# Performance work log

Measured on AMD Instinct MI355X. Metric: run time of the kernel, lower is better.

Reference implementation:

```python
import jax, jax.numpy as jnp
import numpy as np

STRIDE = 8  # window over x[:, max(0, i-stride) : i+1]


def setup_inputs() -> dict:
    key = jax.random.key(0)
    k0, k1, k2, k3, k4 = jax.random.split(key, 5)
    B, T, H = 16, 8192, 256
    x = jax.random.normal(k0, (B, T, H), dtype=jnp.float32)
    s = 1.0 / np.sqrt(H)  # torch nn.Linear default init range
    W_lin = jax.random.uniform(k1, (H, H), jnp.float32, -s, s)
    b_lin = jax.random.uniform(k2, (H,), jnp.float32, -s, s)
    W_mem = jax.random.uniform(k3, (H, H), jnp.float32, -s, s)
    b_mem = jax.random.uniform(k4, (H,), jnp.float32, -s, s)
    return {"x": x, "W_lin": W_lin, "b_lin": b_lin, "W_mem": W_mem, "b_mem": b_mem}


def reference(x, W_lin, b_lin, W_mem, b_mem):
    # x: [B, T, H]; input_dim == hidden_dim so input_lin is None in the original.
    B, T, H = x.shape
    # h = Linear(x)  (torch Linear: x @ W.T + b)
    h = jnp.einsum('bth,oh->bto', x, W_lin) + b_lin
    # Causal sliding-window mean over window [max(0, t-STRIDE), t] via cumsum.
    cs = jnp.cumsum(x, axis=1)                       # [B, T, H]
    idx = jnp.arange(T)
    start = jnp.maximum(0, idx - STRIDE)             # [T]
    prev = jnp.where((start > 0)[None, :, None],
                     cs[:, jnp.maximum(start - 1, 0)], 0.0)
    counts = (idx - start + 1).astype(x.dtype)       # min(t+1, STRIDE+1)
    means = (cs - prev) / counts[None, :, None]      # [B, T, H]
    # memory branch: Linear over window means, batched as one matmul
    mem = jnp.einsum('bth,oh->bto', means, W_mem) + b_mem
    return h + mem
```

## Files before the change

### kernel.cpp

```cpp
#include <hip/hip_runtime.h>
#include <hip/hip_bf16.h>

#define B_ 16
#define T_ 8192
#define H_ 256
#define M_ (B_ * T_)
#define STRIDE_ 8

typedef __bf16 bf16x8 __attribute__((ext_vector_type(8)));
typedef float f32x4 __attribute__((ext_vector_type(4)));

__device__ __forceinline__ unsigned short f2bf(float f) {
  unsigned u = __builtin_bit_cast(unsigned, f);
  u += 0x7fffu + ((u >> 16) & 1u);
  return (unsigned short)(u >> 16);
}

__global__ __launch_bounds__(256) void wcat_kernel(
    const float* __restrict__ Wl, const float* __restrict__ bl,
    const float* __restrict__ Wm, const float* __restrict__ bm,
    unsigned short* __restrict__ Wpk, float* __restrict__ bias) {
  const int e = blockIdx.x * 256 + threadIdx.x;
  const int ks = e >> 13;
  const int n = (e >> 5) & 255;
  const int kk = e & 31;
  const int k = ks * 32 + kk;
  const float w = (k < 256) ? Wl[n * 256 + k] : Wm[n * 256 + (k - 256)];
  Wpk[e] = f2bf(w);
  if (e < 256) bias[e] = bl[e] + bm[e];
}

__global__ __launch_bounds__(256, 3) void fused_kernel(
    const float* __restrict__ x,
    const unsigned short* __restrict__ Wpk,
    const float* __restrict__ bias,
    float* __restrict__ out) {
  __shared__ __align__(16) unsigned short As[2][64 * 64];
  const int tid = threadIdx.x;
  const int m0 = blockIdx.x << 6;
  const int tb0 = m0 & (T_ - 1);
  const int w = tid >> 6;
  const int l = tid & 63;
  const int wc = w << 6;
  const int lm = l & 15;
  const int kc4 = l >> 4;
  const int kq = kc4 << 3;

  const int p = tid & 15, g = tid >> 4;
  const float2* __restrict__ x2 = (const float2*)x;

  f32x4 acc[4][4];
#pragma unroll
  for (int i = 0; i < 4; ++i)
#pragma unroll
    for (int j = 0; j < 4; ++j) acc[i][j] = (f32x4){0.f, 0.f, 0.f, 0.f};

  float2 v[12];
#pragma unroll
  for (int i = 0; i < 12; ++i) {
    const int rl = (g << 2) - 8 + i;
    float2 val = {0.f, 0.f};
    if (tb0 + rl >= 0) val = x2[(size_t)(m0 + rl) * 128 + p];
    v[i] = val;
  }

  for (int it = 0; it < 8; ++it) {
    const int cur = it & 1;
    unsigned* __restrict__ As32 = (unsigned*)As[cur];

    float sx = 0.f, sy = 0.f;
#pragma unroll
    for (int i = 0; i < 8; ++i) { sx += v[i].x; sy += v[i].y; }
#pragma unroll
    for (int rr = 0; rr < 4; ++rr) {
      sx += v[rr + 8].x; sy += v[rr + 8].y;
      const int r = (g << 2) + rr;
      const int t = tb0 + r;
      const float inv =
          (t >= STRIDE_) ? (1.f / 9.f) : __builtin_amdgcn_rcpf((float)(t + 1));
      const unsigned xp =
          (unsigned)f2bf(v[rr + 8].x) | ((unsigned)f2bf(v[rr + 8].y) << 16);
      const unsigned mp =
          (unsigned)f2bf(sx * inv) | ((unsigned)f2bf(sy * inv) << 16);
      const int sw = r & 7;
      As32[r * 32 + (((p >> 2) ^ sw) << 2) + (p & 3)] = xp;
      As32[r * 32 + (((4 + (p >> 2)) ^ sw) << 2) + (p & 3)] = mp;
      sx -= v[rr].x; sy -= v[rr].y;
    }
    __syncthreads();

    const size_t bb0 = ((size_t)it << 13) + (wc + lm) * 32 + kq;
    const size_t bb1 = bb0 + ((size_t)8 << 13);
    bf16x8 b0[4], b1[4], a0[4], a1[4];
#pragma unroll
    for (int j = 0; j < 4; ++j) b0[j] = *(const bf16x8*)&Wpk[bb0 + (j << 9)];
#pragma unroll
    for (int j = 0; j < 4; ++j) b1[j] = *(const bf16x8*)&Wpk[bb1 + (j << 9)];
#pragma unroll
    for (int i = 0; i < 4; ++i) {
      const int R = (i << 4) + lm;
      a0[i] = *(const bf16x8*)&As[cur][R * 64 + ((kc4 ^ (R & 7)) << 3)];
      a1[i] = *(const bf16x8*)&As[cur][R * 64 + (((4 + kc4) ^ (R & 7)) << 3)];
    }
    if (it < 7) {
#pragma unroll
      for (int i = 0; i < 12; ++i) {
        const int rl = (g << 2) - 8 + i;
        float2 val = {0.f, 0.f};
        if (tb0 + rl >= 0)
          val = x2[(size_t)(m0 + rl) * 128 + ((it + 1) << 4) + p];
        v[i] = val;
      }
    }
#pragma unroll
    for (int i = 0; i < 4; ++i)
#pragma unroll
      for (int j = 0; j < 4; ++j)
        acc[i][j] =
            __builtin_amdgcn_mfma_f32_16x16x32_bf16(a0[i], b0[j], acc[i][j], 0, 0, 0);
#pragma unroll
    for (int i = 0; i < 4; ++i)
#pragma unroll
      for (int j = 0; j < 4; ++j)
        acc[i][j] =
            __builtin_amdgcn_mfma_f32_16x16x32_bf16(a1[i], b1[j], acc[i][j], 0, 0, 0);
  }

  const int r0 = (l >> 4) << 2;
#pragma unroll
  for (int j = 0; j < 4; ++j) {
    const int o = wc + (j << 4) + lm;
    const float bs = bias[o];
#pragma unroll
    for (int i = 0; i < 4; ++i) {
      const size_t mr = (size_t)(m0 + (i << 4) + r0);
#pragma unroll
      for (int r = 0; r < 4; ++r) out[(mr + r) * 256 + o] = acc[i][j][r] + bs;
    }
  }
}

extern "C" void kernel_launch(void* const* d_in, const int* in_sizes, int n_in,
                              void* d_out, int out_size, void* d_ws, size_t ws_size,
                              hipStream_t stream) {
  const float* x  = (const float*)d_in[0];
  const float* Wl = (const float*)d_in[1];
  const float* bl = (const float*)d_in[2];
  const float* Wm = (const float*)d_in[3];
  const float* bm = (const float*)d_in[4];
  float* out = (float*)d_out;

  char* ws = (char*)d_ws;
  unsigned short* Wpk = (unsigned short*)ws;
  float* bias = (float*)(ws + (size_t)16 * 256 * 32 * 2);

  wcat_kernel<<<512, 256, 0, stream>>>(Wl, bl, Wm, bm, Wpk, bias);
  fused_kernel<<<2048, 256, 0, stream>>>(x, Wpk, bias, out);
}
```

Measured before the change: 317.2 us.

## Keep weight slices register-resident across multiple row tiles per block

Restructures the fused kernel so each 512-thread block processes eight consecutive 64-row tiles, with each wave holding its 32-column slice of the packed bf16 weights in registers for the whole block. This removes repeated global/L2 loads of the weights per k-step and amortizes them over many tiles, and prefetches the next tile's input across tile boundaries. The grid shrinks to 256 blocks and register pressure rises sharply, which risks reduced occupancy and less latency hiding for the memory-bound x reads and output writes.

```diff
diff --git a/kernel.cpp b/kernel.cpp
--- a/kernel.cpp
+++ b/kernel.cpp
@@ -30,18 +30,17 @@
   if (e < 256) bias[e] = bl[e] + bm[e];
 }
 
-__global__ __launch_bounds__(256, 3) void fused_kernel(
+__global__ __launch_bounds__(512, 2) void fused_kernel(
     const float* __restrict__ x,
     const unsigned short* __restrict__ Wpk,
     const float* __restrict__ bias,
     float* __restrict__ out) {
   __shared__ __align__(16) unsigned short As[2][64 * 64];
   const int tid = threadIdx.x;
-  const int m0 = blockIdx.x << 6;
-  const int tb0 = m0 & (T_ - 1);
+  const int bid = blockIdx.x;
   const int w = tid >> 6;
   const int l = tid & 63;
-  const int wc = w << 6;
+  const int wc = w << 5;
   const int lm = l & 15;
   const int kc4 = l >> 4;
   const int kq = kc4 << 3;
@@ -49,93 +48,114 @@
   const int p = tid & 15, g = tid >> 4;
   const float2* __restrict__ x2 = (const float2*)x;
 
-  f32x4 acc[4][4];
+  bf16x8 breg[16][2];
 #pragma unroll
-  for (int i = 0; i < 4; ++i)
+  for (int ks = 0; ks < 16; ++ks)
 #pragma unroll
-    for (int j = 0; j < 4; ++j) acc[i][j] = (f32x4){0.f, 0.f, 0.f, 0.f};
+    for (int j = 0; j < 2; ++j)
+      breg[ks][j] =
+          *(const bf16x8*)&Wpk[(((ks << 8) + wc + (j << 4) + lm) << 5) + kq];
 
-  float2 v[12];
+  float bsv[2];
 #pragma unroll
-  for (int i = 0; i < 12; ++i) {
-    const int rl = (g << 2) - 8 + i;
-    float2 val = {0.f, 0.f};
-    if (tb0 + rl >= 0) val = x2[(size_t)(m0 + rl) * 128 + p];
-    v[i] = val;
+  for (int j = 0; j < 2; ++j) bsv[j] = bias[wc + (j << 4) + lm];
+
+  float2 v[10];
+  {
+    const int m0 = bid << 9;
+    const int tb0 = m0 & (T_ - 1);
+#pragma unroll
+    for (int i = 0; i < 10; ++i) {
+      const int rl = (g << 1) - 8 + i;
+      float2 val = {0.f, 0.f};
+      if (tb0 + rl >= 0) val = x2[(size_t)(m0 + rl) * 128 + p];
+      v[i] = val;
+    }
   }
 
-  for (int it = 0; it < 8; ++it) {
-    const int cur = it & 1;
-    unsigned* __restrict__ As32 = (unsigned*)As[cur];
+  for (int tile = 0; tile < 8; ++tile) {
+    const int m0 = ((bid << 3) + tile) << 6;
+    const int tb0 = m0 & (T_ - 1);
 
-    float sx = 0.f, sy = 0.f;
-#pragma unroll
-    for (int i = 0; i < 8; ++i) { sx += v[i].x; sy += v[i].y; }
-#pragma unroll
-    for (int rr = 0; rr < 4; ++rr) {
-      sx += v[rr + 8].x; sy += v[rr + 8].y;
-      const int r = (g << 2) + rr;
-      const int t = tb0 + r;
-      const float inv =
-          (t >= STRIDE_) ? (1.f / 9.f) : __builtin_amdgcn_rcpf((float)(t + 1));
-      const unsigned xp =
-          (unsigned)f2bf(v[rr + 8].x) | ((unsigned)f2bf(v[rr + 8].y) << 16);
-      const unsigned mp =
-          (unsigned)f2bf(sx * inv) | ((unsigned)f2bf(sy * inv) << 16);
-      const int sw = r & 7;
-      As32[r * 32 + (((p >> 2) ^ sw) << 2) + (p & 3)] = xp;
-      As32[r * 32 + (((4 + (p >> 2)) ^ sw) << 2) + (p & 3)] = mp;
-      sx -= v[rr].x; sy -= v[rr].y;
-    }
-    __syncthreads();
-
-    const size_t bb0 = ((size_t)it << 13) + (wc + lm) * 32 + kq;
-    const size_t bb1 = bb0 + ((size_t)8 << 13);
-    bf16x8 b0[4], b1[4], a0[4], a1[4];
-#pragma unroll
-    for (int j = 0; j < 4; ++j) b0[j] = *(const bf16x8*)&Wpk[bb0 + (j << 9)];
-#pragma unroll
-    for (int j = 0; j < 4; ++j) b1[j] = *(const bf16x8*)&Wpk[bb1 + (j << 9)];
-#pragma unroll
-    for (int i = 0; i < 4; ++i) {
-      const int R = (i << 4) + lm;
-      a0[i] = *(const bf16x8*)&As[cur][R * 64 + ((kc4 ^ (R & 7)) << 3)];
-      a1[i] = *(const bf16x8*)&As[cur][R * 64 + (((4 + kc4) ^ (R & 7)) << 3)];
-    }
-    if (it < 7) {
-#pragma unroll
-      for (int i = 0; i < 12; ++i) {
-        const int rl = (g << 2) - 8 + i;
-        float2 val = {0.f, 0.f};
-        if (tb0 + rl >= 0)
-          val = x2[(size_t)(m0 + rl) * 128 + ((it + 1) << 4) + p];
-        v[i] = val;
-      }
-    }
+    f32x4 acc[4][2];
 #pragma unroll
     for (int i = 0; i < 4; ++i)
 #pragma unroll
-      for (int j = 0; j < 4; ++j)
-        acc[i][j] =
-            __builtin_amdgcn_mfma_f32_16x16x32_bf16(a0[i], b0[j], acc[i][j], 0, 0, 0);
+      for (int j = 0; j < 2; ++j) acc[i][j] = (f32x4){0.f, 0.f, 0.f, 0.f};
+
 #pragma unroll
-    for (int i = 0; i < 4; ++i)
+    for (int it = 0; it < 8; ++it) {
+      const int cur = it & 1;
+      unsigned* __restrict__ As32 = (unsigned*)As[cur];
+
+      float sx = 0.f, sy = 0.f;
 #pragma unroll
-      for (int j = 0; j < 4; ++j)
-        acc[i][j] =
-            __builtin_amdgcn_mfma_f32_16x16x32_bf16(a1[i], b1[j], acc[i][j], 0, 0, 0);
-  }
+      for (int i = 0; i < 8; ++i) { sx += v[i].x; sy += v[i].y; }
+#pragma unroll
+      for (int rr = 0; rr < 2; ++rr) {
+        sx += v[rr + 8].x; sy += v[rr + 8].y;
+        const int r = (g << 1) + rr;
+        const int t = tb0 + r;
+        const float inv =
+            (t >= STRIDE_) ? (1.f / 9.f) : __builtin_amdgcn_rcpf((float)(t + 1));
+        const unsigned xp =
+            (unsigned)f2bf(v[rr + 8].x) | ((unsigned)f2bf(v[rr + 8].y) << 16);
+        const unsigned mp =
+            (unsigned)f2bf(sx * inv) | ((unsigned)f2bf(sy * inv) << 16);
+        const int sw = r & 7;
+        As32[r * 32 + (((p >> 2) ^ sw) << 2) + (p & 3)] = xp;
+        As32[r * 32 + (((4 + (p >> 2)) ^ sw) << 2) + (p & 3)] = mp;
+        sx -= v[rr].x; sy -= v[rr].y;
+      }
+      __syncthreads();
 
-  const int r0 = (l >> 4) << 2;
+      bf16x8 a0[4], a1[4];
 #pragma unroll
-  for (int j = 0; j < 4; ++j) {
-    const int o = wc + (j << 4) + lm;
-    const float bs = bias[o];
+      for (int i = 0; i < 4; ++i) {
+        const int R = (i << 4) + lm;
+        a0[i] = *(const bf16x8*)&As[cur][R * 64 + ((kc4 ^ (R & 7)) << 3)];
+        a1[i] = *(const bf16x8*)&As[cur][R * 64 + (((4 + kc4) ^ (R & 7)) << 3)];
+      }
+
+      if (it < 7 || tile < 7) {
+        const int nit = (it < 7) ? it + 1 : 0;
+        const int nm0 = (it < 7) ? m0 : m0 + 64;
+        const int ntb0 = nm0 & (T_ - 1);
 #pragma unroll
-    for (int i = 0; i < 4; ++i) {
-      const size_t mr = (size_t)(m0 + (i << 4) + r0);
+        for (int i = 0; i < 10; ++i) {
+          const int rl = (g << 1) - 8 + i;
+          float2 val = {0.f, 0.f};
+          if (ntb0 + rl >= 0)
+            val = x2[(size_t)(nm0 + rl) * 128 + (nit << 4) + p];
+          v[i] = val;
+        }
+      }
+
 #pragma unroll
-      for (int r = 0; r < 4; ++r) out[(mr + r) * 256 + o] = acc[i][j][r] + bs;
+      for (int i = 0; i < 4; ++i)
+#pragma unroll
+        for (int j = 0; j < 2; ++j)
+          acc[i][j] = __builtin_amdgcn_mfma_f32_16x16x32_bf16(
+              a0[i], breg[it][j], acc[i][j], 0, 0, 0);
+#pragma unroll
+      for (int i = 0; i < 4; ++i)
+#pragma unroll
+        for (int j = 0; j < 2; ++j)
+          acc[i][j] = __builtin_amdgcn_mfma_f32_16x16x32_bf16(
+              a1[i], breg[it + 8][j], acc[i][j], 0, 0, 0);
+    }
+
+    const int r0 = (l >> 4) << 2;
+#pragma unroll
+    for (int j = 0; j < 2; ++j) {
+      const int o = wc + (j << 4) + lm;
+      const float bs = bsv[j];
+#pragma unroll
+      for (int i = 0; i < 4; ++i) {
+        const size_t mr = (size_t)(m0 + (i << 4) + r0);
+#pragma unroll
+        for (int r = 0; r < 4; ++r) out[(mr + r) * 256 + o] = acc[i][j][r] + bs;
+      }
     }
   }
 }
@@ -155,5 +175,5 @@
   float* bias = (float*)(ws + (size_t)16 * 256 * 32 * 2);
 
   wcat_kernel<<<512, 256, 0, stream>>>(Wl, bl, Wm, bm, Wpk, bias);
-  fused_kernel<<<2048, 256, 0, stream>>>(x, Wpk, bias, out);
+  fused_kernel<<<256, 512, 0, stream>>>(x, Wpk, bias, out);
 }
```

New measurement: 340.2 us. 7.3% more time.
